# Kernel optimization log

Measured on AMD Instinct MI355X. Metric: run time of the kernel, lower is better.

## Reference

```python
import jax, jax.numpy as jnp
import numpy as np

E = 320000   # num edges / messages
N = 10000    # num target nodes (dim_size)
C = 256      # in_channels == out_channels


def setup_inputs() -> dict:
    key = jax.random.key(0)
    k1, k2, k3, k4, k5, k6 = jax.random.split(key, 6)
    s = 1.0 / np.sqrt(C)  # torch Linear default init bound
    return {
        "from_tensor": jax.random.normal(k1, (E, C), dtype=jnp.float32),
        "to_index": jax.random.randint(k2, (E,), 0, N),
        "dim_size": N,
        "W1": jax.random.uniform(k3, (C, C), jnp.float32, -s, s),
        "b1": jax.random.uniform(k4, (C,), jnp.float32, -s, s),
        "W2": jax.random.uniform(k5, (C, C), jnp.float32, -s, s),
        "b2": jax.random.uniform(k6, (C,), jnp.float32, -s, s),
    }


def reference(from_tensor, to_index, dim_size, W1, b1, W2, b2):
    # InterMessage with transform_scatter=True, num_layers=2, reduction='mean':
    # message = MLP(from_tensor); out = scatter_mean(message, to_index, dim_size)
    m = jax.nn.relu(from_tensor @ W1 + b1)          # [E, C]
    m = jax.nn.relu(m @ W2 + b2)                    # [E, C]
    sums = jax.ops.segment_sum(m, to_index, num_segments=dim_size)  # [N, C]
    cnt = jax.ops.segment_sum(jnp.ones((m.shape[0], 1), m.dtype), to_index,
                              num_segments=dim_size)                # [N, 1]
    # scatter-mean: empty segments produce 0 (matches torch_scatter 'mean')
    return jnp.where(cnt > 0, sums / jnp.maximum(cnt, 1.0), 0.0)
```

## Files before the change

### kernel.cpp

```cpp
#include <hip/hip_runtime.h>

#define NUM_E 320000
#define NUM_N 10000
#define TILE_M 64

typedef __attribute__((ext_vector_type(8))) short bf16x8;
typedef __attribute__((ext_vector_type(4))) float f32x4;

__device__ __forceinline__ short f2bf(float f) {
  unsigned u = __builtin_bit_cast(unsigned, f);
  u += 0x7FFFu + ((u >> 16) & 1u);
  return (short)(u >> 16);
}

__global__ void prep_w(const float* __restrict__ W1, const float* __restrict__ W2,
                       short* __restrict__ Wp) {
  int gid = blockIdx.x * 256 + threadIdx.x;
  const float* W = (gid & 8192) ? W2 : W1;
  int r = gid & 8191;
  short* dst = Wp + (gid >> 13) * 65536 + r * 8;
  int j = r >> 9;
  int s = (r >> 6) & 7;
  int lane = r & 63;
  int n = j * 16 + (lane & 15);
  int k0 = s * 32 + (lane >> 4) * 8;
  short tmp[8];
#pragma unroll
  for (int e = 0; e < 8; ++e) tmp[e] = f2bf(W[(k0 + e) * 256 + n]);
#pragma unroll
  for (int e = 0; e < 8; ++e) dst[e] = tmp[e];
}

__global__ __launch_bounds__(256, 2) void fused_mlp_scatter(
    const float* __restrict__ X, const int* __restrict__ idx,
    const short* __restrict__ Wp1, const short* __restrict__ Wp2,
    const float* __restrict__ b1, const float* __restrict__ b2,
    float* __restrict__ out, int* __restrict__ cnt) {
  __shared__ short Xl[TILE_M][264];
  __shared__ int idxl[TILE_M];

  const int tid = threadIdx.x;
  const int wave = tid >> 6;
  const int lane = tid & 63;
  const int q = lane >> 4;
  const int m = lane & 15;
  const int row0 = blockIdx.x * TILE_M;

  for (int i = tid; i < TILE_M * 64; i += 256) {
    int r = i >> 6, c4 = i & 63;
    float4 v = reinterpret_cast<const float4*>(X + (size_t)(row0 + r) * 256)[c4];
    unsigned long long packed =
        (unsigned long long)(unsigned short)f2bf(v.x) |
        ((unsigned long long)(unsigned short)f2bf(v.y) << 16) |
        ((unsigned long long)(unsigned short)f2bf(v.z) << 32) |
        ((unsigned long long)(unsigned short)f2bf(v.w) << 48);
    *reinterpret_cast<unsigned long long*>(&Xl[r][c4 * 4]) = packed;
  }
  if (tid < TILE_M) {
    int ix = idx[row0 + tid];
    idxl[tid] = ix;
    atomicAdd(&cnt[ix], 1);
  }
  __syncthreads();

  f32x4 acc[4][4];
#pragma unroll
  for (int mi = 0; mi < 4; ++mi)
#pragma unroll
    for (int nj = 0; nj < 4; ++nj) acc[mi][nj] = (f32x4)0.0f;

#pragma unroll
  for (int s = 0; s < 8; ++s) {
    bf16x8 a[4], b[4];
#pragma unroll
    for (int mi = 0; mi < 4; ++mi)
      a[mi] = *reinterpret_cast<const bf16x8*>(&Xl[mi * 16 + m][s * 32 + q * 8]);
#pragma unroll
    for (int nj = 0; nj < 4; ++nj)
      b[nj] = *reinterpret_cast<const bf16x8*>(
          Wp1 + (size_t)(((wave * 4 + nj) * 8 + s) * 64 + lane) * 8);
#pragma unroll
    for (int mi = 0; mi < 4; ++mi)
#pragma unroll
      for (int nj = 0; nj < 4; ++nj)
        acc[mi][nj] = __builtin_amdgcn_mfma_f32_16x16x32_bf16(a[mi], b[nj],
                                                              acc[mi][nj], 0, 0, 0);
  }
  __syncthreads();

  float bias1[4];
#pragma unroll
  for (int nj = 0; nj < 4; ++nj) bias1[nj] = b1[wave * 64 + nj * 16 + m];
#pragma unroll
  for (int mi = 0; mi < 4; ++mi)
#pragma unroll
    for (int nj = 0; nj < 4; ++nj)
#pragma unroll
      for (int r4 = 0; r4 < 4; ++r4) {
        float v = acc[mi][nj][r4] + bias1[nj];
        v = fmaxf(v, 0.0f);
        Xl[mi * 16 + q * 4 + r4][wave * 64 + nj * 16 + m] = f2bf(v);
      }
  __syncthreads();

#pragma unroll
  for (int mi = 0; mi < 4; ++mi)
#pragma unroll
    for (int nj = 0; nj < 4; ++nj) acc[mi][nj] = (f32x4)0.0f;

#pragma unroll
  for (int s = 0; s < 8; ++s) {
    bf16x8 a[4], b[4];
#pragma unroll
    for (int mi = 0; mi < 4; ++mi)
      a[mi] = *reinterpret_cast<const bf16x8*>(&Xl[mi * 16 + m][s * 32 + q * 8]);
#pragma unroll
    for (int nj = 0; nj < 4; ++nj)
      b[nj] = *reinterpret_cast<const bf16x8*>(
          Wp2 + (size_t)(((wave * 4 + nj) * 8 + s) * 64 + lane) * 8);
#pragma unroll
    for (int mi = 0; mi < 4; ++mi)
#pragma unroll
      for (int nj = 0; nj < 4; ++nj)
        acc[mi][nj] = __builtin_amdgcn_mfma_f32_16x16x32_bf16(a[mi], b[nj],
                                                              acc[mi][nj], 0, 0, 0);
  }

  float bias2[4];
#pragma unroll
  for (int nj = 0; nj < 4; ++nj) bias2[nj] = b2[wave * 64 + nj * 16 + m];
#pragma unroll
  for (int mi = 0; mi < 4; ++mi)
#pragma unroll
    for (int r4 = 0; r4 < 4; ++r4) {
      int rr = mi * 16 + q * 4 + r4;
      int node = idxl[rr];
#pragma unroll
      for (int nj = 0; nj < 4; ++nj) {
        int cc = wave * 64 + nj * 16 + m;
        float v = fmaxf(acc[mi][nj][r4] + bias2[nj], 0.0f);
        atomicAdd(&out[node * 256 + cc], v);
      }
    }
}

__global__ void finalize(float* __restrict__ out, const int* __restrict__ cnt) {
  int i = blockIdx.x * 256 + threadIdx.x;
  if (i >= NUM_N * 64) return;
  int n = i >> 6;
  float c = (float)cnt[n];
  float inv = c > 0.0f ? 1.0f / c : 0.0f;
  float4 v = reinterpret_cast<float4*>(out)[i];
  v.x *= inv; v.y *= inv; v.z *= inv; v.w *= inv;
  reinterpret_cast<float4*>(out)[i] = v;
}

extern "C" void kernel_launch(void* const* d_in, const int* in_sizes, int n_in,
                              void* d_out, int out_size, void* d_ws, size_t ws_size,
                              hipStream_t stream) {
  const float* X   = (const float*)d_in[0];
  const int*   idx = (const int*)d_in[1];
  const float* W1  = (const float*)d_in[3];
  const float* b1  = (const float*)d_in[4];
  const float* W2  = (const float*)d_in[5];
  const float* b2  = (const float*)d_in[6];
  float* out = (float*)d_out;

  short* Wp  = (short*)d_ws;
  int*   cnt = (int*)((char*)d_ws + 2 * 65536 * 2);

  hipMemsetAsync(out, 0, (size_t)NUM_N * 256 * sizeof(float), stream);
  hipMemsetAsync(cnt, 0, NUM_N * sizeof(int), stream);

  prep_w<<<64, 256, 0, stream>>>(W1, W2, Wp);
  fused_mlp_scatter<<<NUM_E / TILE_M, 256, 0, stream>>>(
      X, idx, Wp, Wp + 65536, b1, b2, out, cnt);
  finalize<<<(NUM_N * 64 + 255) / 256, 256, 0, stream>>>(out, cnt);
}
```

Measured before the change: 671.5 us.

## Sort edges by target node and reduce segments in shared memory before atomics

Adds a counting-sort pipeline (histogram, single-block scan, scatter) that orders edge ids by target node. The MLP kernel then gathers X rows in sorted order, stages the output tile in shared memory, and has each thread run-length-sum one column across the 64 rows. It issues one pre-scaled atomicAdd per segment instead of one per element, and the finalize kernel is dropped. The gathered X reads lose contiguity, and three extra small launches are added. The skip of zero partial sums is harmless because a zero contribution changes nothing.

```diff
diff --git a/kernel.cpp b/kernel.cpp
--- a/kernel.cpp
+++ b/kernel.cpp
@@ -2,7 +2,6 @@
 
 #define NUM_E 320000
 #define NUM_N 10000
-#define TILE_M 64
 
 typedef __attribute__((ext_vector_type(8))) short bf16x8;
 typedef __attribute__((ext_vector_type(4))) float f32x4;
@@ -31,24 +30,85 @@
   for (int e = 0; e < 8; ++e) dst[e] = tmp[e];
 }
 
-__global__ __launch_bounds__(256, 2) void fused_mlp_scatter(
+__global__ void hist_k(const int* __restrict__ idx, int* __restrict__ cnt) {
+  int e = blockIdx.x * 256 + threadIdx.x;
+  if (e < NUM_E) atomicAdd(&cnt[idx[e]], 1);
+}
+
+__global__ void scan_k(const int* __restrict__ cnt, int* __restrict__ fill,
+                       float* __restrict__ inv) {
+  __shared__ int part[256];
+  int t = threadIdx.x;
+  int base = t * 40;
+  int local[40];
+  int s = 0;
+#pragma unroll
+  for (int i = 0; i < 40; ++i) {
+    int n = base + i;
+    int c = (n < NUM_N) ? cnt[n] : 0;
+    local[i] = s;
+    s += c;
+  }
+  part[t] = s;
+  __syncthreads();
+  for (int off = 1; off < 256; off <<= 1) {
+    int tmp = 0;
+    if (t >= off) tmp = part[t - off];
+    __syncthreads();
+    if (t >= off) part[t] += tmp;
+    __syncthreads();
+  }
+  int ebase = (t == 0) ? 0 : part[t - 1];
+#pragma unroll
+  for (int i = 0; i < 40; ++i) {
+    int n = base + i;
+    if (n < NUM_N) {
+      fill[n] = ebase + local[i];
+      int c = cnt[n];
+      inv[n] = (c > 0) ? 1.0f / (float)c : 0.0f;
+    }
+  }
+}
+
+__global__ void scatter_k(const int* __restrict__ idx, int* __restrict__ fill,
+                          int* __restrict__ sorted) {
+  int e = blockIdx.x * 256 + threadIdx.x;
+  if (e < NUM_E) {
+    int ix = idx[e];
+    int pos = atomicAdd(&fill[ix], 1);
+    sorted[pos] = e;
+  }
+}
+
+__global__ __launch_bounds__(256, 2) void fused_mlp_gather(
     const float* __restrict__ X, const int* __restrict__ idx,
+    const int* __restrict__ sorted,
     const short* __restrict__ Wp1, const short* __restrict__ Wp2,
     const float* __restrict__ b1, const float* __restrict__ b2,
-    float* __restrict__ out, int* __restrict__ cnt) {
-  __shared__ short Xl[TILE_M][264];
-  __shared__ int idxl[TILE_M];
+    const float* __restrict__ inv, float* __restrict__ out) {
+  __shared__ __align__(16) float smem[64 * 260];
+  short (*Xl)[264] = reinterpret_cast<short(*)[264]>(smem);
+  float (*Yout)[260] = reinterpret_cast<float(*)[260]>(smem);
+  __shared__ int idxl[64];
+  __shared__ int se[64];
 
   const int tid = threadIdx.x;
   const int wave = tid >> 6;
   const int lane = tid & 63;
   const int q = lane >> 4;
   const int m = lane & 15;
-  const int row0 = blockIdx.x * TILE_M;
-
-  for (int i = tid; i < TILE_M * 64; i += 256) {
+  const int row0 = blockIdx.x * 64;
+
+  if (tid < 64) {
+    int e = sorted[row0 + tid];
+    se[tid] = e;
+    idxl[tid] = idx[e];
+  }
+  __syncthreads();
+
+  for (int i = tid; i < 64 * 64; i += 256) {
     int r = i >> 6, c4 = i & 63;
-    float4 v = reinterpret_cast<const float4*>(X + (size_t)(row0 + r) * 256)[c4];
+    float4 v = reinterpret_cast<const float4*>(X + (size_t)se[r] * 256)[c4];
     unsigned long long packed =
         (unsigned long long)(unsigned short)f2bf(v.x) |
         ((unsigned long long)(unsigned short)f2bf(v.y) << 16) |
@@ -56,11 +116,6 @@
         ((unsigned long long)(unsigned short)f2bf(v.w) << 48);
     *reinterpret_cast<unsigned long long*>(&Xl[r][c4 * 4]) = packed;
   }
-  if (tid < TILE_M) {
-    int ix = idx[row0 + tid];
-    idxl[tid] = ix;
-    atomicAdd(&cnt[ix], 1);
-  }
   __syncthreads();
 
   f32x4 acc[4][4];
@@ -97,8 +152,7 @@
     for (int nj = 0; nj < 4; ++nj)
 #pragma unroll
       for (int r4 = 0; r4 < 4; ++r4) {
-        float v = acc[mi][nj][r4] + bias1[nj];
-        v = fmaxf(v, 0.0f);
+        float v = fmaxf(acc[mi][nj][r4] + bias1[nj], 0.0f);
         Xl[mi * 16 + q * 4 + r4][wave * 64 + nj * 16 + m] = f2bf(v);
       }
   __syncthreads();
@@ -125,6 +179,7 @@
         acc[mi][nj] = __builtin_amdgcn_mfma_f32_16x16x32_bf16(a[mi], b[nj],
                                                               acc[mi][nj], 0, 0, 0);
   }
+  __syncthreads();
 
   float bias2[4];
 #pragma unroll
@@ -132,27 +187,25 @@
 #pragma unroll
   for (int mi = 0; mi < 4; ++mi)
 #pragma unroll
-    for (int r4 = 0; r4 < 4; ++r4) {
-      int rr = mi * 16 + q * 4 + r4;
-      int node = idxl[rr];
-#pragma unroll
-      for (int nj = 0; nj < 4; ++nj) {
-        int cc = wave * 64 + nj * 16 + m;
-        float v = fmaxf(acc[mi][nj][r4] + bias2[nj], 0.0f);
-        atomicAdd(&out[node * 256 + cc], v);
-      }
+    for (int nj = 0; nj < 4; ++nj)
+#pragma unroll
+      for (int r4 = 0; r4 < 4; ++r4)
+        Yout[mi * 16 + q * 4 + r4][wave * 64 + nj * 16 + m] =
+            fmaxf(acc[mi][nj][r4] + bias2[nj], 0.0f);
+  __syncthreads();
+
+  float run = 0.0f;
+  int prev = idxl[0];
+  for (int r = 0; r < 64; ++r) {
+    int node = idxl[r];
+    if (node != prev) {
+      if (run != 0.0f) atomicAdd(&out[(size_t)prev * 256 + tid], run * inv[prev]);
+      run = 0.0f;
+      prev = node;
     }
-}
-
-__global__ void finalize(float* __restrict__ out, const int* __restrict__ cnt) {
-  int i = blockIdx.x * 256 + threadIdx.x;
-  if (i >= NUM_N * 64) return;
-  int n = i >> 6;
-  float c = (float)cnt[n];
-  float inv = c > 0.0f ? 1.0f / c : 0.0f;
-  float4 v = reinterpret_cast<float4*>(out)[i];
-  v.x *= inv; v.y *= inv; v.z *= inv; v.w *= inv;
-  reinterpret_cast<float4*>(out)[i] = v;
+    run += Yout[r][tid];
+  }
+  if (run != 0.0f) atomicAdd(&out[(size_t)prev * 256 + tid], run * inv[prev]);
 }
 
 extern "C" void kernel_launch(void* const* d_in, const int* in_sizes, int n_in,
@@ -166,14 +219,20 @@
   const float* b2  = (const float*)d_in[6];
   float* out = (float*)d_out;
 
-  short* Wp  = (short*)d_ws;
-  int*   cnt = (int*)((char*)d_ws + 2 * 65536 * 2);
+  char* ws = (char*)d_ws;
+  short* Wp     = (short*)(ws);
+  int*   cnt    = (int*)(ws + 262144);
+  int*   fill   = (int*)(ws + 303104);
+  float* inv    = (float*)(ws + 344064);
+  int*   sorted = (int*)(ws + 385024);
 
   hipMemsetAsync(out, 0, (size_t)NUM_N * 256 * sizeof(float), stream);
   hipMemsetAsync(cnt, 0, NUM_N * sizeof(int), stream);
 
   prep_w<<<64, 256, 0, stream>>>(W1, W2, Wp);
-  fused_mlp_scatter<<<NUM_E / TILE_M, 256, 0, stream>>>(
-      X, idx, Wp, Wp + 65536, b1, b2, out, cnt);
-  finalize<<<(NUM_N * 64 + 255) / 256, 256, 0, stream>>>(out, cnt);
-}
+  hist_k<<<(NUM_E + 255) / 256, 256, 0, stream>>>(idx, cnt);
+  scan_k<<<1, 256, 0, stream>>>(cnt, fill, inv);
+  scatter_k<<<(NUM_E + 255) / 256, 256, 0, stream>>>(idx, fill, sorted);
+  fused_mlp_gather<<<NUM_E / 64, 256, 0, stream>>>(
+      X, idx, sorted, Wp, Wp + 65536, b1, b2, inv, out);
+}
```

Result: no change. 665.0 us (-1.0%).
